# Kernel optimization log

Measured on AMD Instinct MI355X. Metric: run time of the kernel, lower is better.

The kernel has to match this reference:

```python
import jax, jax.numpy as jnp
import numpy as np

B, N, D, V, Y = 4, 2048, 300, 50000, 20000
MAX_REL = 10
LN_EPS = 1e-5


def setup_inputs() -> dict:
    key = jax.random.key(0)
    k1, k2, k3, k4, k5 = jax.random.split(key, 5)
    M_s = jax.random.randint(k1, (B, N), 0, V, dtype=jnp.int64)
    s = 1.0 / np.sqrt(D)
    E_v = jax.random.normal(k2, (V, D), dtype=jnp.float32) * s
    E_v = E_v.at[0].set(0.0)  # padding_idx=0
    E_y = jax.random.normal(k3, (Y, D), dtype=jnp.float32) * s
    E_y = E_y.at[0].set(0.0)
    W_A = jax.random.normal(k4, (D, D), dtype=jnp.float32) * s
    W_O = jax.random.normal(k5, (D, D), dtype=jnp.float32) * s
    gamma = jnp.ones((D,), dtype=jnp.float32)
    beta = jnp.zeros((D,), dtype=jnp.float32)
    return {"M_s": M_s, "E_v": E_v, "E_y": E_y, "W_A": W_A, "W_O": W_O,
            "gamma": gamma, "beta": beta}


def reference(M_s, E_v, E_y, W_A, W_O, gamma, beta):
    # Embedding lookup (dropout is identity in eval / p=0)
    X = E_v[M_s]                                   # [B, N, D]
    Q = X                                          # self-attention mode (v_q=None)
    # weights = Q @ W_A @ X^T
    QW = jnp.einsum('bnd,de->bne', Q, W_A)         # [B, N, D]
    weights = jnp.einsum('bne,bme->bnm', QW, X)    # [B, N, N]
    # relative-distance bias (clipped |i-j|)
    r = jnp.arange(N)
    dist = jnp.clip(jnp.abs(r[None, :] - r[:, None]), 0, MAX_REL).astype(weights.dtype)
    weights = weights - dist
    # padding mask over context (key) positions
    mask = (M_s != 0)                              # [B, N]
    weights = jnp.where(mask[:, None, :], weights, -jnp.inf)
    A = jax.nn.softmax(weights, axis=-1)           # [B, N, N]
    # contextualized query + output projection
    Q_c = jnp.einsum('bnm,bmd->bnd', A, X) @ W_O   # [B, N, D]
    # residual + layernorm over D
    H = Q_c + Q
    mu = jnp.mean(H, axis=-1, keepdims=True)
    var = jnp.mean((H - mu) ** 2, axis=-1, keepdims=True)
    Hn = (H - mu) * jax.lax.rsqrt(var + LN_EPS) * gamma + beta
    # vocab projection over senses
    y_logits = Hn @ E_y.T                          # [B, N, Y]
    return y_logits, A
```

## Files before the change

### kernel.cpp

```cpp
#include <hip/hip_runtime.h>
#include <hip/hip_bf16.h>

#define B_ 4
#define N_ 2048
#define D_ 300
#define Y_ 20000
#define ROWS (B_*N_)

typedef __attribute__((ext_vector_type(8))) short bf16x8;
typedef __attribute__((ext_vector_type(4))) float f32x4;

__device__ __forceinline__ unsigned short f2bf(float f) {
  unsigned u = __float_as_uint(f);
  unsigned r = (u + 0x7FFFu + ((u >> 16) & 1u)) >> 16;
  return (unsigned short)r;
}

__device__ __forceinline__ void gl_lds16(const unsigned short* g, unsigned short* l) {
  __builtin_amdgcn_global_load_lds(
      (const __attribute__((address_space(1))) void*)g,
      (__attribute__((address_space(3))) void*)l, 16, 0, 0);
}

__global__ __launch_bounds__(256) void k_gather_pack(const int* __restrict__ M_s,
    const float* __restrict__ E_v, float* __restrict__ X,
    unsigned short* __restrict__ Xp) {
  __shared__ float xs[320];
  int row = blockIdx.x, tid = threadIdx.x;
  int tok = M_s[row];
  const float* src = E_v + (size_t)tok * D_;
  for (int d = tid; d < 320; d += 256) xs[d] = (d < D_) ? src[d] : 0.f;
  __syncthreads();
  float* dst = X + (size_t)row * D_;
  for (int d = tid; d < D_; d += 256) dst[d] = xs[d];
  if (tid < 40) {
    int kt = tid >> 2, j = tid & 3;
    int tile = row >> 7, fb = (row >> 4) & 7, rl = row & 15;
    unsigned short v[8];
    #pragma unroll
    for (int e = 0; e < 8; ++e) v[e] = f2bf(xs[kt*32 + j*8 + e]);
    size_t off_ = ((size_t)(tile*10 + kt))*4096 + fb*512 + rl*8 + j*128;
    ushort4* o = (ushort4*)&Xp[off_];
    o[0] = make_ushort4(v[0],v[1],v[2],v[3]);
    o[1] = make_ushort4(v[4],v[5],v[6],v[7]);
  }
}

__global__ __launch_bounds__(256) void k_pack(const float* __restrict__ src,
    unsigned short* __restrict__ dst, int nrows, int ncols, int KT) {
  int chunk = blockIdx.x;
  int tile = chunk / KT, kt = chunk - tile*KT;
  size_t obase = (size_t)chunk * 4096;
  #pragma unroll
  for (int p = 0; p < 2; ++p) {
    int idx = p*256 + threadIdx.x;
    int fb = idx >> 6, l = idx & 63;
    int row = tile*128 + fb*16 + (l & 15);
    int gk = kt*32 + (l >> 4)*8;
    unsigned short v[8];
    #pragma unroll
    for (int e = 0; e < 8; ++e) {
      int k = gk + e;
      float f = (row < nrows && k < ncols) ? src[(size_t)row*ncols + k] : 0.f;
      v[e] = f2bf(f);
    }
    ushort4* o = (ushort4*)&dst[obase + (size_t)idx*8];
    o[0] = make_ushort4(v[0],v[1],v[2],v[3]);
    o[1] = make_ushort4(v[4],v[5],v[6],v[7]);
  }
}

__global__ __launch_bounds__(256) void k_packT(const float* __restrict__ src,
    unsigned short* __restrict__ dst, int src_rows, int src_cols, int KT,
    size_t src_bstride, size_t dst_bchunks) {
  __shared__ float ls[32*133];
  int chunk = blockIdx.x, b = blockIdx.y, tid = threadIdx.x;
  const float* s = src + (size_t)b * src_bstride;
  unsigned short* d = dst + ((size_t)b * dst_bchunks + chunk) * 4096;
  int tile = chunk / KT, kt = chunk - tile*KT;
  int c0 = tile*128, k0 = kt*32;
  for (int i = tid; i < 4096; i += 256) {
    int r = i >> 7, c = i & 127;
    int sr = k0 + r, sc = c0 + c;
    ls[r*133 + c] = (sr < src_rows && sc < src_cols) ? s[(size_t)sr*src_cols + sc] : 0.f;
  }
  __syncthreads();
  #pragma unroll
  for (int p = 0; p < 2; ++p) {
    int idx = p*256 + tid;
    int fb = idx >> 6, l = idx & 63;
    int r = fb*16 + (l & 15);
    int kl = (l >> 4)*8;
    unsigned short v[8];
    #pragma unroll
    for (int e = 0; e < 8; ++e) v[e] = f2bf(ls[(kl + e)*133 + r]);
    ushort4* o = (ushort4*)&d[(size_t)idx*8];
    o[0] = make_ushort4(v[0],v[1],v[2],v[3]);
    o[1] = make_ushort4(v[4],v[5],v[6],v[7]);
  }
}

template<int EPI, bool NT, bool SWZ>
__global__ __launch_bounds__(512, 4) void k_gemm256(
    const unsigned short* __restrict__ Ap, const unsigned short* __restrict__ Bp,
    float* __restrict__ out, const int* __restrict__ Ms,
    int MTB, int NTB, int ncols)
{
  __shared__ __align__(16) union {
    unsigned short bstage[10][4096];
    float epi[64*132];
  } sm;
  int nt, mt, z;
  if (SWZ) {
    int wg = blockIdx.x;
    int cpx = (MTB*NTB) >> 3;
    int swz = (wg & 7)*cpx + (wg >> 3);
    mt = swz % MTB; nt = swz / MTB; z = 0;
  } else { nt = blockIdx.x; mt = blockIdx.y; z = blockIdx.z; }
  const int tid = threadIdx.x;
  const int wave = tid >> 6, lane = tid & 63;
  const int wm = wave >> 1, wn = wave & 1;
  const int mtile2 = (z*MTB + mt)*2 + (wm >> 1);
  const unsigned short* Ab = Ap + (size_t)mtile2 * 10 * 4096;
  const unsigned short* Bb = Bp + (size_t)(z*NTB + nt) * 10 * 4096;

  #pragma unroll
  for (int kt = 0; kt < 10; ++kt)
    gl_lds16(Bb + kt*4096 + wave*512 + lane*8, &sm.bstage[kt][wave*512]);

  const unsigned short* ga = Ab + ((wm & 1)*4)*512 + lane*8;
  __syncthreads();

  f32x4 acc[4][4] = {};
  #pragma unroll
  for (int kt = 0; kt < 10; ++kt) {
    bf16x8 a4[4], b4[4];
    #pragma unroll
    for (int i = 0; i < 4; ++i)
      a4[i] = *(const bf16x8*)(ga + kt*4096 + i*512);
    #pragma unroll
    for (int i = 0; i < 4; ++i)
      b4[i] = *(const bf16x8*)&sm.bstage[kt][(wn*4 + i)*512 + lane*8];
    #pragma unroll
    for (int mi = 0; mi < 4; ++mi)
      #pragma unroll
      for (int ni = 0; ni < 4; ++ni)
        acc[mi][ni] = __builtin_amdgcn_mfma_f32_16x16x32_bf16(
            a4[mi], b4[ni], acc[mi][ni], 0, 0, 0);
  }
  __syncthreads();

  const int lr0 = (lane >> 4) << 2;
  const int lc0 = wn*64 + (lane & 15);
  const size_t growbase = ((size_t)(z*MTB + mt)) << 8;
  #pragma unroll
  for (int h = 0; h < 4; ++h) {
    if (wm == h) {
      int tok[4];
      if (EPI == 1) {
        #pragma unroll
        for (int ni = 0; ni < 4; ++ni)
          tok[ni] = Ms[z*N_ + (nt<<7) + lc0 + ni*16];
      }
      #pragma unroll
      for (int mi = 0; mi < 4; ++mi) {
        #pragma unroll
        for (int ni = 0; ni < 4; ++ni) {
          int col = lc0 + ni*16;
          #pragma unroll
          for (int r = 0; r < 4; ++r) {
            int row = lr0 + mi*16 + r;
            float v = acc[mi][ni][r];
            if (EPI == 1) {
              int rb = (mt<<8) + h*64 + row;
              int gc = (nt<<7) + col;
              int dd = rb - gc; if (dd < 0) dd = -dd; if (dd > 10) dd = 10;
              v -= (float)dd;
              if (tok[ni] == 0) v = -3.0e38f;
            }
            sm.epi[row*132 + col] = v;
          }
        }
      }
    }
    __syncthreads();
    {
      const int r0 = tid >> 5;
      const int c4 = (tid & 31) << 2;
      const int gc = (nt << 7) + c4;
      #pragma unroll
      for (int rr = r0; rr < 64; rr += 16) {
        size_t grow = growbase + h*64 + rr;
        if (gc + 3 < ncols) {
          f32x4 v = *(const f32x4*)&sm.epi[rr*132 + c4];
          if (NT) __builtin_nontemporal_store(v, (f32x4*)&out[grow*(size_t)ncols + gc]);
          else    *(f32x4*)&out[grow*(size_t)ncols + gc] = v;
        } else {
          #pragma unroll
          for (int e = 0; e < 4; ++e) {
            int c = gc + e;
            if (c < ncols) {
              float v = sm.epi[rr*132 + c4 + e];
              if (NT) __builtin_nontemporal_store(v, &out[grow*(size_t)ncols + c]);
              else    out[grow*(size_t)ncols + c] = v;
            }
          }
        }
      }
    }
    __syncthreads();
  }
}

template<int EPI, bool NT, bool PACKOUT, bool SWZ>
__global__ __launch_bounds__(256) void k_gemm10(
    const unsigned short* __restrict__ Ap, const unsigned short* __restrict__ Bp,
    float* __restrict__ out, unsigned short* __restrict__ outp,
    const float* __restrict__ resid, const int* __restrict__ Ms,
    int KTd, int MTB, int NTB, int ncols)
{
  __shared__ __align__(16) union {
    unsigned short bstage[10][4096];
    float epi[64*132];
  } sm;
  int nt, mt, z;
  if (SWZ) {
    int nwg = MTB * NTB;
    int wg = blockIdx.x;
    int cpx = nwg >> 3;
    int swz = (wg & 7) * cpx + (wg >> 3);
    mt = swz % MTB; nt = swz / MTB; z = 0;
  } else {
    nt = blockIdx.x; mt = blockIdx.y; z = blockIdx.z;
  }
  const int tid = threadIdx.x;
  const int wave = tid >> 6, lane = tid & 63;
  const int wm = wave >> 1, wn = wave & 1;
  const unsigned short* Ab = Ap + (size_t)(z*MTB + mt) * 10 * 4096;
  const unsigned short* Bb = Bp + (size_t)(z*NTB + nt) * 10 * 4096;

  #pragma unroll
  for (int kt = 0; kt < 10; ++kt) {
    const unsigned short* gb = Bb + kt*4096 + wave*1024 + lane*8;
    unsigned short* lb = &sm.bstage[kt][wave*1024];
    gl_lds16(gb,       lb);
    gl_lds16(gb + 512, lb + 512);
  }

  const unsigned short* ga = Ab + (wm*4)*512 + lane*8;
  bf16x8 aA[4], aB[4];
  #pragma unroll
  for (int i = 0; i < 4; ++i) aA[i] = *(const bf16x8*)(ga + 0*4096 + i*512);
  #pragma unroll
  for (int i = 0; i < 4; ++i) aB[i] = *(const bf16x8*)(ga + 1*4096 + i*512);

  __syncthreads();

  f32x4 acc[4][4] = {};
  auto mfma_step = [&](int kt, const bf16x8* a) {
    bf16x8 bfr[4];
    #pragma unroll
    for (int i = 0; i < 4; ++i)
      bfr[i] = *(const bf16x8*)&sm.bstage[kt][(wn*4 + i)*512 + lane*8];
    #pragma unroll
    for (int mi = 0; mi < 4; ++mi)
      #pragma unroll
      for (int ni = 0; ni < 4; ++ni)
        acc[mi][ni] = __builtin_amdgcn_mfma_f32_16x16x32_bf16(
            a[mi], bfr[ni], acc[mi][ni], 0, 0, 0);
  };
  auto loadA = [&](int kt, bf16x8* d) {
    #pragma unroll
    for (int i = 0; i < 4; ++i) d[i] = *(const bf16x8*)(ga + kt*4096 + i*512);
  };

  #pragma unroll
  for (int kt = 0; kt < 10; kt += 2) {
    mfma_step(kt, aA);
    if (kt + 2 < 10) loadA(kt + 2, aA);
    mfma_step(kt + 1, aB);
    if (kt + 3 < 10) loadA(kt + 3, aB);
  }

  __syncthreads();

  const int lr0 = (lane >> 4) << 2;
  const int lc0 = wn*64 + (lane & 15);
  const size_t growbase = ((size_t)(z*MTB + mt)) << 7;
  #pragma unroll
  for (int h = 0; h < 2; ++h) {
    if (wm == h) {
      int tok[4];
      if (EPI == 1) {
        #pragma unroll
        for (int ni = 0; ni < 4; ++ni)
          tok[ni] = Ms[z*N_ + (nt<<7) + lc0 + ni*16];
      }
      #pragma unroll
      for (int mi = 0; mi < 4; ++mi) {
        #pragma unroll
        for (int ni = 0; ni < 4; ++ni) {
          int col = lc0 + ni*16;
          #pragma unroll
          for (int r = 0; r < 4; ++r) {
            int row = lr0 + mi*16 + r;
            float v = acc[mi][ni][r];
            if (EPI == 1) {
              int rb = (mt<<7) + h*64 + row;
              int gc = (nt<<7) + col;
              int dd = rb - gc; if (dd < 0) dd = -dd; if (dd > 10) dd = 10;
              v -= (float)dd;
              if (tok[ni] == 0) v = -3.0e38f;
            }
            sm.epi[row*132 + col] = v;
          }
        }
      }
    }
    __syncthreads();
    if (PACKOUT) {
      int prow = tid >> 2, pktq = tid & 3;
      int ktd = nt*4 + pktq;
      if (ktd < KTd) {
        int grl = h*64 + prow;
        int fb = grl >> 4, rl = grl & 15;
        size_t cbase = ((size_t)((z*MTB + mt)*KTd + ktd))*4096 + fb*512 + rl*8;
        #pragma unroll
        for (int oct = 0; oct < 4; ++oct) {
          unsigned short v[8];
          #pragma unroll
          for (int e = 0; e < 8; ++e)
            v[e] = f2bf(sm.epi[prow*132 + pktq*32 + oct*8 + e]);
          ushort4* o = (ushort4*)&outp[cbase + oct*128];
          o[0] = make_ushort4(v[0],v[1],v[2],v[3]);
          o[1] = make_ushort4(v[4],v[5],v[6],v[7]);
        }
      }
    } else {
      const int r0 = tid >> 5;
      const int c4 = (tid & 31) << 2;
      const int gc = (nt << 7) + c4;
      #pragma unroll
      for (int rr = r0; rr < 64; rr += 8) {
        size_t grow = growbase + h*64 + rr;
        if (gc + 3 < ncols) {
          f32x4 v = *(const f32x4*)&sm.epi[rr*132 + c4];
          if (EPI == 2) v += *(const f32x4*)&resid[grow*(size_t)ncols + gc];
          if (NT) __builtin_nontemporal_store(v, (f32x4*)&out[grow*(size_t)ncols + gc]);
          else    *(f32x4*)&out[grow*(size_t)ncols + gc] = v;
        } else {
          #pragma unroll
          for (int e = 0; e < 4; ++e) {
            int c = gc + e;
            if (c < ncols) {
              float v = sm.epi[rr*132 + c4 + e];
              if (EPI == 2) v += resid[grow*(size_t)ncols + c];
              if (NT) __builtin_nontemporal_store(v, &out[grow*(size_t)ncols + c]);
              else    out[grow*(size_t)ncols + c] = v;
            }
          }
        }
      }
    }
    __syncthreads();
  }
}

__global__ __launch_bounds__(256) void k_gemm64(
    const unsigned short* __restrict__ Ap, const unsigned short* __restrict__ Bp,
    unsigned short* __restrict__ outp, int KT, int KTd, int MTB, int NTB)
{
  __shared__ __align__(16) union {
    unsigned short stage[2][2][4096];
    float epi[64*132];
  } sm;
  const int nt = blockIdx.x, mt = blockIdx.y, z = blockIdx.z;
  const int tid = threadIdx.x;
  const int wave = tid >> 6, lane = tid & 63;
  const int wm = wave >> 1, wn = wave & 1;
  const unsigned short* Ab = Ap + (size_t)(z*MTB + mt) * KT * 4096;
  const unsigned short* Bb = Bp + (size_t)(z*NTB + nt) * KT * 4096;
  f32x4 acc[4][4] = {};

  auto stage = [&](int s, int kt) {
    const unsigned short* ga = Ab + kt*4096 + wave*1024 + lane*8;
    const unsigned short* gb = Bb + kt*4096 + wave*1024 + lane*8;
    unsigned short* la = &sm.stage[s][0][wave*1024];
    unsigned short* lb = &sm.stage[s][1][wave*1024];
    gl_lds16(ga,       la);
    gl_lds16(ga + 512, la + 512);
    gl_lds16(gb,       lb);
    gl_lds16(gb + 512, lb + 512);
  };

  stage(0, 0);
  __syncthreads();
  for (int kt = 0; kt < KT; ++kt) {
    int cur = kt & 1;
    if (kt + 1 < KT) stage(cur ^ 1, kt + 1);
    bf16x8 af[4], bfr[4];
    #pragma unroll
    for (int i = 0; i < 4; ++i)
      af[i] = *(const bf16x8*)&sm.stage[cur][0][(wm*4 + i)*512 + lane*8];
    #pragma unroll
    for (int i = 0; i < 4; ++i)
      bfr[i] = *(const bf16x8*)&sm.stage[cur][1][(wn*4 + i)*512 + lane*8];
    #pragma unroll
    for (int mi = 0; mi < 4; ++mi)
      #pragma unroll
      for (int ni = 0; ni < 4; ++ni)
        acc[mi][ni] = __builtin_amdgcn_mfma_f32_16x16x32_bf16(
            af[mi], bfr[ni], acc[mi][ni], 0, 0, 0);
    __syncthreads();
  }

  const int lr0 = (lane >> 4) << 2;
  const int lc0 = wn*64 + (lane & 15);
  #pragma unroll
  for (int h = 0; h < 2; ++h) {
    if (wm == h) {
      #pragma unroll
      for (int mi = 0; mi < 4; ++mi)
        #pragma unroll
        for (int ni = 0; ni < 4; ++ni) {
          int col = lc0 + ni*16;
          #pragma unroll
          for (int r = 0; r < 4; ++r)
            sm.epi[(lr0 + mi*16 + r)*132 + col] = acc[mi][ni][r];
        }
    }
    __syncthreads();
    {
      int prow = tid >> 2, pktq = tid & 3;
      int ktd = nt*4 + pktq;
      if (ktd < KTd) {
        int grl = h*64 + prow;
        int fb = grl >> 4, rl = grl & 15;
        size_t cbase = ((size_t)((z*MTB + mt)*KTd + ktd))*4096 + fb*512 + rl*8;
        #pragma unroll
        for (int oct = 0; oct < 4; ++oct) {
          unsigned short v[8];
          #pragma unroll
          for (int e = 0; e < 8; ++e)
            v[e] = f2bf(sm.epi[prow*132 + pktq*32 + oct*8 + e]);
          ushort4* o = (ushort4*)&outp[cbase + oct*128];
          o[0] = make_ushort4(v[0],v[1],v[2],v[3]);
          o[1] = make_ushort4(v[4],v[5],v[6],v[7]);
        }
      }
    }
    __syncthreads();
  }
}

__global__ __launch_bounds__(256) void k_softmax(float* __restrict__ S,
    unsigned short* __restrict__ Apk) {
  __shared__ float w[N_];
  __shared__ float redm[4], reds[4];
  int row = blockIdx.x, tid = threadIdx.x;
  float* sr = S + (size_t)row * N_;
  f32x4 v0 = ((const f32x4*)sr)[tid];
  f32x4 v1 = ((const f32x4*)sr)[tid + 256];
  float vmax = fmaxf(fmaxf(fmaxf(v0.x, v0.y), fmaxf(v0.z, v0.w)),
                     fmaxf(fmaxf(v1.x, v1.y), fmaxf(v1.z, v1.w)));
  #pragma unroll
  for (int off = 32; off; off >>= 1) vmax = fmaxf(vmax, __shfl_down(vmax, off, 64));
  if ((tid & 63) == 0) redm[tid >> 6] = vmax;
  __syncthreads();
  vmax = fmaxf(fmaxf(redm[0], redm[1]), fmaxf(redm[2], redm[3]));
  f32x4 e0, e1;
  e0.x = __expf(v0.x - vmax); e0.y = __expf(v0.y - vmax);
  e0.z = __expf(v0.z - vmax); e0.w = __expf(v0.w - vmax);
  e1.x = __expf(v1.x - vmax); e1.y = __expf(v1.y - vmax);
  e1.z = __expf(v1.z - vmax); e1.w = __expf(v1.w - vmax);
  ((f32x4*)w)[tid] = e0;
  ((f32x4*)w)[tid + 256] = e1;
  float vsum = (e0.x + e0.y + e0.z + e0.w) + (e1.x + e1.y + e1.z + e1.w);
  #pragma unroll
  for (int off = 32; off; off >>= 1) vsum += __shfl_down(vsum, off, 64);
  if ((tid & 63) == 0) reds[tid >> 6] = vsum;
  __syncthreads();
  float inv = 1.f / ((reds[0] + reds[1]) + (reds[2] + reds[3]));
  f32x4 o0 = e0 * inv, o1 = e1 * inv;
  __builtin_nontemporal_store(o0, &((f32x4*)sr)[tid]);
  __builtin_nontemporal_store(o1, &((f32x4*)sr)[tid + 256]);
  int kt = tid >> 2, j = tid & 3;
  int m0 = kt*32 + j*8;
  int fb = (row >> 4) & 7, rl = row & 15;
  unsigned short v[8];
  #pragma unroll
  for (int e = 0; e < 8; ++e) v[e] = f2bf(w[m0 + e] * inv);
  size_t off_ = ((size_t)((row >> 7)*64 + kt))*4096 + fb*512 + rl*8 + j*128;
  ushort4* o = (ushort4*)&Apk[off_];
  o[0] = make_ushort4(v[0],v[1],v[2],v[3]);
  o[1] = make_ushort4(v[4],v[5],v[6],v[7]);
}

__global__ __launch_bounds__(320) void k_ln_pack(const float* __restrict__ H,
    const float* __restrict__ gamma, const float* __restrict__ beta,
    unsigned short* __restrict__ Hp) {
  __shared__ float red[5];
  __shared__ float hs[320];
  int row = blockIdx.x, tid = threadIdx.x;
  float h = (tid < D_) ? H[(size_t)row*D_ + tid] : 0.f;
  float s = h;
  #pragma unroll
  for (int off = 32; off; off >>= 1) s += __shfl_down(s, off, 64);
  if ((tid & 63) == 0) red[tid >> 6] = s;
  __syncthreads();
  float mu = (red[0]+red[1]+red[2]+red[3]+red[4]) * (1.f/(float)D_);
  float dv = (tid < D_) ? (h - mu) : 0.f;
  float s2 = dv * dv;
  #pragma unroll
  for (int off = 32; off; off >>= 1) s2 += __shfl_down(s2, off, 64);
  __syncthreads();
  if ((tid & 63) == 0) red[tid >> 6] = s2;
  __syncthreads();
  float var = (red[0]+red[1]+red[2]+red[3]+red[4]) * (1.f/(float)D_);
  float rstd = rsqrtf(var + 1e-5f);
  hs[tid] = (tid < D_) ? (dv * rstd * gamma[tid] + beta[tid]) : 0.f;
  __syncthreads();
  if (tid < 40) {
    int kt = tid >> 2, j = tid & 3;
    int tile = row >> 7, fb = (row >> 4) & 7, rl = row & 15;
    unsigned short v[8];
    #pragma unroll
    for (int e = 0; e < 8; ++e) v[e] = f2bf(hs[kt*32 + j*8 + e]);
    size_t off_ = ((size_t)(tile*10 + kt))*4096 + fb*512 + rl*8 + j*128;
    ushort4* o = (ushort4*)&Hp[off_];
    o[0] = make_ushort4(v[0],v[1],v[2],v[3]);
    o[1] = make_ushort4(v[4],v[5],v[6],v[7]);
  }
}

extern "C" void kernel_launch(void* const* d_in, const int* in_sizes, int n_in,
                              void* d_out, int out_size, void* d_ws, size_t ws_size,
                              hipStream_t stream) {
  const int*   M_s   = (const int*)d_in[0];
  const float* E_v   = (const float*)d_in[1];
  const float* E_y   = (const float*)d_in[2];
  const float* W_A   = (const float*)d_in[3];
  const float* W_O   = (const float*)d_in[4];
  const float* gamma = (const float*)d_in[5];
  const float* beta  = (const float*)d_in[6];

  float* Yl = (float*)d_out;
  float* A  = Yl + (size_t)ROWS * Y_;

  float* X  = (float*)d_ws;
  float* QW = X  + (size_t)ROWS * D_;
  float* H  = QW + (size_t)ROWS * D_;
  unsigned short* Ep = (unsigned short*)(H + (size_t)ROWS * D_);
  unsigned short* Hpk = (unsigned short*)X;

  unsigned short* scr = (unsigned short*)(Yl + 100000000ull);
  unsigned short* Xp  = scr;
  unsigned short* QWp = Xp  + 2621440;
  unsigned short* Wap = QWp + 2621440;
  unsigned short* Wop = Wap + 122880;
  unsigned short* XTp = Wop + 122880;
  unsigned short* Cp  = XTp + 3145728;
  unsigned short* Apk = Cp  + 2621440;

  k_gather_pack<<<ROWS, 256, 0, stream>>>(M_s, E_v, X, Xp);
  k_packT <<<dim3(3*10,1), 256, 0, stream>>>(W_A, Wap, D_, D_, 10, 0, 0);
  k_gemm10<0,false,true,false><<<dim3(3,64,1), 256, 0, stream>>>(
      Xp, Wap, nullptr, QWp, nullptr, nullptr, 10, 64, 3, D_);
  k_gemm256<1,false,false><<<dim3(16,8,4), 512, 0, stream>>>(
      QWp, Xp, A, M_s, 8, 16, N_);
  k_softmax<<<ROWS, 256, 0, stream>>>(A, Apk);
  k_packT <<<dim3(3*64,4), 256, 0, stream>>>(X, XTp, N_, D_, 64, (size_t)N_*D_, 192);
  k_gemm64<<<dim3(3,16,4), 256, 0, stream>>>(Apk, XTp, Cp, 64, 10, 16, 3);
  k_packT <<<dim3(3*10,1), 256, 0, stream>>>(W_O, Wop, D_, D_, 10, 0, 0);
  k_gemm10<2,false,false,false><<<dim3(3,64,1), 256, 0, stream>>>(
      Cp, Wop, H, nullptr, X, nullptr, 0, 64, 3, D_);
  k_ln_pack<<<ROWS, 320, 0, stream>>>(H, gamma, beta, Hpk);
  k_pack  <<<157*10, 256, 0, stream>>>(E_y, Ep, Y_, D_, 10);
  k_gemm256<0,true,true><<<dim3(157*32,1,1), 512, 0, stream>>>(
      Hpk, Ep, Yl, nullptr, 32, 157, Y_);
}
```

Measured before the change: 373.7 us.

## Merge weight-packing launches and widen GEMM epilogue staging to fewer passes

Folds the E_y bf16 packing into the gather kernel and packs W_A and W_O in a single launch, removing two kernel launches. The GEMM epilogues now stage 128 rows in LDS instead of 64, so the 4-pass and 2-pass store loops become 2 passes and 1 pass with fewer barriers. The larger epilogue buffer raises LDS use, which may cap occupancy in the 10-tile GEMM kernels.

```diff
diff --git a/kernel.cpp b/kernel.cpp
--- a/kernel.cpp
+++ b/kernel.cpp
@@ -24,7 +24,8 @@
 
 __global__ __launch_bounds__(256) void k_gather_pack(const int* __restrict__ M_s,
     const float* __restrict__ E_v, float* __restrict__ X,
-    unsigned short* __restrict__ Xp) {
+    unsigned short* __restrict__ Xp, const float* __restrict__ Ey,
+    unsigned short* __restrict__ Ep) {
   __shared__ float xs[320];
   int row = blockIdx.x, tid = threadIdx.x;
   int tok = M_s[row];
@@ -44,27 +45,54 @@
     o[0] = make_ushort4(v[0],v[1],v[2],v[3]);
     o[1] = make_ushort4(v[4],v[5],v[6],v[7]);
   }
-}
-
-__global__ __launch_bounds__(256) void k_pack(const float* __restrict__ src,
-    unsigned short* __restrict__ dst, int nrows, int ncols, int KT) {
-  int chunk = blockIdx.x;
-  int tile = chunk / KT, kt = chunk - tile*KT;
-  size_t obase = (size_t)chunk * 4096;
+  if (row < 157*10) {
+    int tile = row / 10, kt = row - tile*10;
+    size_t obase = (size_t)row * 4096;
+    #pragma unroll
+    for (int p = 0; p < 2; ++p) {
+      int idx = p*256 + tid;
+      int fb = idx >> 6, l = idx & 63;
+      int rr = tile*128 + fb*16 + (l & 15);
+      int gk = kt*32 + (l >> 4)*8;
+      unsigned short v[8];
+      #pragma unroll
+      for (int e = 0; e < 8; ++e) {
+        int k = gk + e;
+        float f = (rr < Y_ && k < D_) ? Ey[(size_t)rr*D_ + k] : 0.f;
+        v[e] = f2bf(f);
+      }
+      ushort4* o = (ushort4*)&Ep[obase + (size_t)idx*8];
+      o[0] = make_ushort4(v[0],v[1],v[2],v[3]);
+      o[1] = make_ushort4(v[4],v[5],v[6],v[7]);
+    }
+  }
+}
+
+__global__ __launch_bounds__(256) void k_packTW(const float* __restrict__ s0,
+    unsigned short* __restrict__ d0, const float* __restrict__ s1,
+    unsigned short* __restrict__ d1) {
+  __shared__ float ls[32*133];
+  int chunk = blockIdx.x, tid = threadIdx.x;
+  const float* s = blockIdx.y ? s1 : s0;
+  unsigned short* d = (blockIdx.y ? d1 : d0) + (size_t)chunk * 4096;
+  int tile = chunk / 10, kt = chunk - tile*10;
+  int c0 = tile*128, k0 = kt*32;
+  for (int i = tid; i < 4096; i += 256) {
+    int r = i >> 7, c = i & 127;
+    int sr = k0 + r, sc = c0 + c;
+    ls[r*133 + c] = (sr < D_ && sc < D_) ? s[(size_t)sr*D_ + sc] : 0.f;
+  }
+  __syncthreads();
   #pragma unroll
   for (int p = 0; p < 2; ++p) {
-    int idx = p*256 + threadIdx.x;
+    int idx = p*256 + tid;
     int fb = idx >> 6, l = idx & 63;
-    int row = tile*128 + fb*16 + (l & 15);
-    int gk = kt*32 + (l >> 4)*8;
+    int r = fb*16 + (l & 15);
+    int kl = (l >> 4)*8;
     unsigned short v[8];
     #pragma unroll
-    for (int e = 0; e < 8; ++e) {
-      int k = gk + e;
-      float f = (row < nrows && k < ncols) ? src[(size_t)row*ncols + k] : 0.f;
-      v[e] = f2bf(f);
-    }
-    ushort4* o = (ushort4*)&dst[obase + (size_t)idx*8];
+    for (int e = 0; e < 8; ++e) v[e] = f2bf(ls[(kl + e)*133 + r]);
+    ushort4* o = (ushort4*)&d[(size_t)idx*8];
     o[0] = make_ushort4(v[0],v[1],v[2],v[3]);
     o[1] = make_ushort4(v[4],v[5],v[6],v[7]);
   }
@@ -108,7 +136,7 @@
 {
   __shared__ __align__(16) union {
     unsigned short bstage[10][4096];
-    float epi[64*132];
+    float epi[128*132];
   } sm;
   int nt, mt, z;
   if (SWZ) {
@@ -154,14 +182,15 @@
   const int lc0 = wn*64 + (lane & 15);
   const size_t growbase = ((size_t)(z*MTB + mt)) << 8;
   #pragma unroll
-  for (int h = 0; h < 4; ++h) {
-    if (wm == h) {
+  for (int hp = 0; hp < 2; ++hp) {
+    if ((wm >> 1) == hp) {
       int tok[4];
       if (EPI == 1) {
         #pragma unroll
         for (int ni = 0; ni < 4; ++ni)
           tok[ni] = Ms[z*N_ + (nt<<7) + lc0 + ni*16];
       }
+      const int rbase = (wm & 1)*64;
       #pragma unroll
       for (int mi = 0; mi < 4; ++mi) {
         #pragma unroll
@@ -169,10 +198,10 @@
           int col = lc0 + ni*16;
           #pragma unroll
           for (int r = 0; r < 4; ++r) {
-            int row = lr0 + mi*16 + r;
+            int row = rbase + lr0 + mi*16 + r;
             float v = acc[mi][ni][r];
             if (EPI == 1) {
-              int rb = (mt<<8) + h*64 + row;
+              int rb = (mt<<8) + hp*128 + row;
               int gc = (nt<<7) + col;
               int dd = rb - gc; if (dd < 0) dd = -dd; if (dd > 10) dd = 10;
               v -= (float)dd;
@@ -189,8 +218,8 @@
       const int c4 = (tid & 31) << 2;
       const int gc = (nt << 7) + c4;
       #pragma unroll
-      for (int rr = r0; rr < 64; rr += 16) {
-        size_t grow = growbase + h*64 + rr;
+      for (int rr = r0; rr < 128; rr += 16) {
+        size_t grow = growbase + hp*128 + rr;
         if (gc + 3 < ncols) {
           f32x4 v = *(const f32x4*)&sm.epi[rr*132 + c4];
           if (NT) __builtin_nontemporal_store(v, (f32x4*)&out[grow*(size_t)ncols + gc]);
@@ -221,7 +250,7 @@
 {
   __shared__ __align__(16) union {
     unsigned short bstage[10][4096];
-    float epi[64*132];
+    float epi[128*132];
   } sm;
   int nt, mt, z;
   if (SWZ) {
@@ -287,82 +316,81 @@
   const int lr0 = (lane >> 4) << 2;
   const int lc0 = wn*64 + (lane & 15);
   const size_t growbase = ((size_t)(z*MTB + mt)) << 7;
-  #pragma unroll
-  for (int h = 0; h < 2; ++h) {
-    if (wm == h) {
-      int tok[4];
-      if (EPI == 1) {
+  {
+    int tok[4];
+    if (EPI == 1) {
+      #pragma unroll
+      for (int ni = 0; ni < 4; ++ni)
+        tok[ni] = Ms[z*N_ + (nt<<7) + lc0 + ni*16];
+    }
+    const int rbase = wm*64;
+    #pragma unroll
+    for (int mi = 0; mi < 4; ++mi) {
+      #pragma unroll
+      for (int ni = 0; ni < 4; ++ni) {
+        int col = lc0 + ni*16;
         #pragma unroll
-        for (int ni = 0; ni < 4; ++ni)
-          tok[ni] = Ms[z*N_ + (nt<<7) + lc0 + ni*16];
-      }
-      #pragma unroll
-      for (int mi = 0; mi < 4; ++mi) {
-        #pragma unroll
-        for (int ni = 0; ni < 4; ++ni) {
-          int col = lc0 + ni*16;
-          #pragma unroll
-          for (int r = 0; r < 4; ++r) {
-            int row = lr0 + mi*16 + r;
-            float v = acc[mi][ni][r];
-            if (EPI == 1) {
-              int rb = (mt<<7) + h*64 + row;
-              int gc = (nt<<7) + col;
-              int dd = rb - gc; if (dd < 0) dd = -dd; if (dd > 10) dd = 10;
-              v -= (float)dd;
-              if (tok[ni] == 0) v = -3.0e38f;
-            }
-            sm.epi[row*132 + col] = v;
+        for (int r = 0; r < 4; ++r) {
+          int row = rbase + lr0 + mi*16 + r;
+          float v = acc[mi][ni][r];
+          if (EPI == 1) {
+            int rb = (mt<<7) + row;
+            int gc = (nt<<7) + col;
+            int dd = rb - gc; if (dd < 0) dd = -dd; if (dd > 10) dd = 10;
+            v -= (float)dd;
+            if (tok[ni] == 0) v = -3.0e38f;
           }
+          sm.epi[row*132 + col] = v;
         }
       }
     }
-    __syncthreads();
-    if (PACKOUT) {
-      int prow = tid >> 2, pktq = tid & 3;
+  }
+  __syncthreads();
+  if (PACKOUT) {
+    #pragma unroll
+    for (int p = 0; p < 2; ++p) {
+      int row = p*64 + (tid >> 2), pktq = tid & 3;
       int ktd = nt*4 + pktq;
       if (ktd < KTd) {
-        int grl = h*64 + prow;
-        int fb = grl >> 4, rl = grl & 15;
+        int fb = row >> 4, rl = row & 15;
         size_t cbase = ((size_t)((z*MTB + mt)*KTd + ktd))*4096 + fb*512 + rl*8;
         #pragma unroll
         for (int oct = 0; oct < 4; ++oct) {
           unsigned short v[8];
           #pragma unroll
           for (int e = 0; e < 8; ++e)
-            v[e] = f2bf(sm.epi[prow*132 + pktq*32 + oct*8 + e]);
+            v[e] = f2bf(sm.epi[row*132 + pktq*32 + oct*8 + e]);
           ushort4* o = (ushort4*)&outp[cbase + oct*128];
           o[0] = make_ushort4(v[0],v[1],v[2],v[3]);
           o[1] = make_ushort4(v[4],v[5],v[6],v[7]);
         }
       }
-    } else {
-      const int r0 = tid >> 5;
-      const int c4 = (tid & 31) << 2;
-      const int gc = (nt << 7) + c4;
-      #pragma unroll
-      for (int rr = r0; rr < 64; rr += 8) {
-        size_t grow = growbase + h*64 + rr;
-        if (gc + 3 < ncols) {
-          f32x4 v = *(const f32x4*)&sm.epi[rr*132 + c4];
-          if (EPI == 2) v += *(const f32x4*)&resid[grow*(size_t)ncols + gc];
-          if (NT) __builtin_nontemporal_store(v, (f32x4*)&out[grow*(size_t)ncols + gc]);
-          else    *(f32x4*)&out[grow*(size_t)ncols + gc] = v;
-        } else {
-          #pragma unroll
-          for (int e = 0; e < 4; ++e) {
-            int c = gc + e;
-            if (c < ncols) {
-              float v = sm.epi[rr*132 + c4 + e];
-              if (EPI == 2) v += resid[grow*(size_t)ncols + c];
-              if (NT) __builtin_nontemporal_store(v, &out[grow*(size_t)ncols + c]);
-              else    out[grow*(size_t)ncols + c] = v;
-            }
+    }
+  } else {
+    const int r0 = tid >> 5;
+    const int c4 = (tid & 31) << 2;
+    const int gc = (nt << 7) + c4;
+    #pragma unroll
+    for (int rr = r0; rr < 128; rr += 8) {
+      size_t grow = growbase + rr;
+      if (gc + 3 < ncols) {
+        f32x4 v = *(const f32x4*)&sm.epi[rr*132 + c4];
+        if (EPI == 2) v += *(const f32x4*)&resid[grow*(size_t)ncols + gc];
+        if (NT) __builtin_nontemporal_store(v, (f32x4*)&out[grow*(size_t)ncols + gc]);
+        else    *(f32x4*)&out[grow*(size_t)ncols + gc] = v;
+      } else {
+        #pragma unroll
+        for (int e = 0; e < 4; ++e) {
+          int c = gc + e;
+          if (c < ncols) {
+            float v = sm.epi[rr*132 + c4 + e];
+            if (EPI == 2) v += resid[grow*(size_t)ncols + c];
+            if (NT) __builtin_nontemporal_store(v, &out[grow*(size_t)ncols + c]);
+            else    out[grow*(size_t)ncols + c] = v;
           }
         }
       }
     }
-    __syncthreads();
   }
 }
 
@@ -372,7 +400,7 @@
 {
   __shared__ __align__(16) union {
     unsigned short stage[2][2][4096];
-    float epi[64*132];
+    float epi[128*132];
   } sm;
   const int nt = blockIdx.x, mt = blockIdx.y, z = blockIdx.z;
   const int tid = threadIdx.x;
@@ -416,40 +444,37 @@
 
   const int lr0 = (lane >> 4) << 2;
   const int lc0 = wn*64 + (lane & 15);
-  #pragma unroll
-  for (int h = 0; h < 2; ++h) {
-    if (wm == h) {
-      #pragma unroll
-      for (int mi = 0; mi < 4; ++mi)
+  {
+    const int rbase = wm*64;
+    #pragma unroll
+    for (int mi = 0; mi < 4; ++mi)
+      #pragma unroll
+      for (int ni = 0; ni < 4; ++ni) {
+        int col = lc0 + ni*16;
         #pragma unroll
-        for (int ni = 0; ni < 4; ++ni) {
-          int col = lc0 + ni*16;
-          #pragma unroll
-          for (int r = 0; r < 4; ++r)
-            sm.epi[(lr0 + mi*16 + r)*132 + col] = acc[mi][ni][r];
-        }
-    }
-    __syncthreads();
-    {
-      int prow = tid >> 2, pktq = tid & 3;
-      int ktd = nt*4 + pktq;
-      if (ktd < KTd) {
-        int grl = h*64 + prow;
-        int fb = grl >> 4, rl = grl & 15;
-        size_t cbase = ((size_t)((z*MTB + mt)*KTd + ktd))*4096 + fb*512 + rl*8;
+        for (int r = 0; r < 4; ++r)
+          sm.epi[(rbase + lr0 + mi*16 + r)*132 + col] = acc[mi][ni][r];
+      }
+  }
+  __syncthreads();
+  #pragma unroll
+  for (int p = 0; p < 2; ++p) {
+    int row = p*64 + (tid >> 2), pktq = tid & 3;
+    int ktd = nt*4 + pktq;
+    if (ktd < KTd) {
+      int fb = row >> 4, rl = row & 15;
+      size_t cbase = ((size_t)((z*MTB + mt)*KTd + ktd))*4096 + fb*512 + rl*8;
+      #pragma unroll
+      for (int oct = 0; oct < 4; ++oct) {
+        unsigned short v[8];
         #pragma unroll
-        for (int oct = 0; oct < 4; ++oct) {
-          unsigned short v[8];
-          #pragma unroll
-          for (int e = 0; e < 8; ++e)
-            v[e] = f2bf(sm.epi[prow*132 + pktq*32 + oct*8 + e]);
-          ushort4* o = (ushort4*)&outp[cbase + oct*128];
-          o[0] = make_ushort4(v[0],v[1],v[2],v[3]);
-          o[1] = make_ushort4(v[4],v[5],v[6],v[7]);
-        }
-      }
-    }
-    __syncthreads();
+        for (int e = 0; e < 8; ++e)
+          v[e] = f2bf(sm.epi[row*132 + pktq*32 + oct*8 + e]);
+        ushort4* o = (ushort4*)&outp[cbase + oct*128];
+        o[0] = make_ushort4(v[0],v[1],v[2],v[3]);
+        o[1] = make_ushort4(v[4],v[5],v[6],v[7]);
+      }
+    }
   }
 }
 
@@ -562,8 +587,8 @@
   unsigned short* Cp  = XTp + 3145728;
   unsigned short* Apk = Cp  + 2621440;
 
-  k_gather_pack<<<ROWS, 256, 0, stream>>>(M_s, E_v, X, Xp);
-  k_packT <<<dim3(3*10,1), 256, 0, stream>>>(W_A, Wap, D_, D_, 10, 0, 0);
+  k_gather_pack<<<ROWS, 256, 0, stream>>>(M_s, E_v, X, Xp, E_y, Ep);
+  k_packTW<<<dim3(30, 2), 256, 0, stream>>>(W_A, Wap, W_O, Wop);
   k_gemm10<0,false,true,false><<<dim3(3,64,1), 256, 0, stream>>>(
       Xp, Wap, nullptr, QWp, nullptr, nullptr, 10, 64, 3, D_);
   k_gemm256<1,false,false><<<dim3(16,8,4), 512, 0, stream>>>(
@@ -571,11 +596,9 @@
   k_softmax<<<ROWS, 256, 0, stream>>>(A, Apk);
   k_packT <<<dim3(3*64,4), 256, 0, stream>>>(X, XTp, N_, D_, 64, (size_t)N_*D_, 192);
   k_gemm64<<<dim3(3,16,4), 256, 0, stream>>>(Apk, XTp, Cp, 64, 10, 16, 3);
-  k_packT <<<dim3(3*10,1), 256, 0, stream>>>(W_O, Wop, D_, D_, 10, 0, 0);
   k_gemm10<2,false,false,false><<<dim3(3,64,1), 256, 0, stream>>>(
       Cp, Wop, H, nullptr, X, nullptr, 0, 64, 3, D_);
   k_ln_pack<<<ROWS, 320, 0, stream>>>(H, gamma, beta, Hpk);
-  k_pack  <<<157*10, 256, 0, stream>>>(E_y, Ep, Y_, D_, 10);
   k_gemm256<0,true,true><<<dim3(157*32,1,1), 512, 0, stream>>>(
       Hpk, Ep, Yl, nullptr, 32, 157, Y_);
 }
```

After: 362.7 us. -3.0%, faster.
